# Optimization experiments

Hardware: AMD Instinct MI355X
Metric: run time of the kernel (lower is better)

The kernel has to match this reference:

```python
import jax, jax.numpy as jnp
import numpy as np

B, T, D_MODEL = 2, 2048, 2048
N_HEAD, N_KV, HD = 32, 8, 64


def _rope_tables(T, hd, base=10000.0):
    # standard rotary tables, (T, hd) with frequencies repeated over both halves
    inv_freq = 1.0 / (base ** (np.arange(0, hd // 2, dtype=np.float32) / (hd // 2)))
    t = np.arange(T, dtype=np.float32)
    freqs = np.outer(t, inv_freq)            # (T, hd/2)
    emb = np.concatenate([freqs, freqs], axis=-1)  # (T, hd)
    return jnp.asarray(np.cos(emb)), jnp.asarray(np.sin(emb))


def setup_inputs() -> dict:
    key = jax.random.key(0)
    ks = jax.random.split(key, 5)
    cos, sin = _rope_tables(T, HD)
    s = 0.02
    return {
        "x": jax.random.normal(ks[0], (B, T, D_MODEL), jnp.float32),
        "cos": cos,
        "sin": sin,
        "Wq": jax.random.normal(ks[1], (N_HEAD * HD, D_MODEL), jnp.float32) * s,
        "Wk": jax.random.normal(ks[2], (N_KV * HD, D_MODEL), jnp.float32) * s,
        "Wv": jax.random.normal(ks[3], (N_KV * HD, D_MODEL), jnp.float32) * s,
        "Wo": jax.random.normal(ks[4], (D_MODEL, N_HEAD * HD), jnp.float32) * s,
    }


def _apply_rope(x, cos, sin):
    # x: (B, H, T, D); cos/sin: (T, D)
    D = x.shape[-1]
    x1, x2 = x[..., : D // 2], x[..., D // 2 :]
    rot = jnp.concatenate([-x2, x1], axis=-1)
    c = cos[: x.shape[-2]][None, None]
    s = sin[: x.shape[-2]][None, None]
    return x * c + rot * s


def reference(x, cos, sin, Wq, Wk, Wv, Wo):
    Bv, Tv, _ = x.shape
    q = (x @ Wq.T).reshape(Bv, Tv, N_HEAD, HD).transpose(0, 2, 1, 3)  # (B,H,T,D)
    k = (x @ Wk.T).reshape(Bv, Tv, N_KV, HD).transpose(0, 2, 1, 3)    # (B,Hkv,T,D)
    v = (x @ Wv.T).reshape(Bv, Tv, N_KV, HD).transpose(0, 2, 1, 3)
    q = _apply_rope(q, cos, sin)
    k = _apply_rope(k, cos, sin)
    repeat = N_HEAD // N_KV
    if repeat > 1:
        k = jnp.repeat(k, repeat, axis=1)
        v = jnp.repeat(v, repeat, axis=1)
    scale = 1.0 / jnp.sqrt(jnp.float32(HD)).astype(x.dtype)
    scores = jnp.einsum("bhqd,bhkd->bhqk", q, k) * scale
    causal = jnp.tril(jnp.ones((Tv, Tv), dtype=bool))
    scores = jnp.where(causal[None, None], scores, jnp.finfo(scores.dtype).min)
    attn = jax.nn.softmax(scores, axis=-1)
    out = jnp.einsum("bhqk,bhkd->bhqd", attn, v)
    out = out.transpose(0, 2, 1, 3).reshape(Bv, Tv, N_HEAD * HD)
    return out @ Wo.T
```

## Files before the change

kernel.cpp:

```cpp
#include <hip/hip_runtime.h>
#include <stdint.h>

#define B_SZ 2
#define T_SEQ 2048
#define DM 2048
#define NH 32
#define NKV 8
#define HD 64
#define QKV_W 3072

typedef unsigned short u16;
typedef __bf16 bf16x8 __attribute__((ext_vector_type(8)));
typedef float floatx4 __attribute__((ext_vector_type(4)));

__device__ __forceinline__ float bf2f(u16 u) {
  union { unsigned u; float f; } v; v.u = ((unsigned)u) << 16; return v.f;
}
__device__ __forceinline__ u16 f2bf(float f) {
  union { float f; unsigned u; } v; v.f = f;
  unsigned r = v.u + 0x7fff + ((v.u >> 16) & 1);
  return (u16)(r >> 16);
}
__device__ __forceinline__ unsigned pk2bf(float hi, float lo) {
  return __builtin_amdgcn_perm(__float_as_uint(hi), __float_as_uint(lo), 0x07060302u);
}
__device__ __forceinline__ float fexp2(float x) {
#if __has_builtin(__builtin_amdgcn_exp2f)
  return __builtin_amdgcn_exp2f(x);
#else
  return exp2f(x);
#endif
}

__device__ __forceinline__ void gld_lds16(const void* g, void* l) {
  __builtin_amdgcn_global_load_lds(
      (const __attribute__((address_space(1))) unsigned int*)g,
      (__attribute__((address_space(3))) unsigned int*)l, 16, 0, 0);
}

__global__ __launch_bounds__(256) void conv_kernel(
    const float* __restrict__ src, u16* __restrict__ dst, int n4)
{
  int i = blockIdx.x * 256 + threadIdx.x;
  int stride = gridDim.x * 256;
  for (; i < n4; i += stride) {
    float4 v = ((const float4*)src)[i];
    ushort4 o;
    o.x = f2bf(v.x); o.y = f2bf(v.y); o.z = f2bf(v.z); o.w = f2bf(v.w);
    ((ushort4*)dst)[i] = o;
  }
}

__global__ __launch_bounds__(256) void gemm_qkv_kernel(
    const u16* __restrict__ A, const u16* __restrict__ Bt,
    u16* __restrict__ C)
{
  __shared__ __align__(16) u16 sA[128 * 32];
  __shared__ __align__(16) u16 sB[128 * 32];

  const int n0 = blockIdx.x * 128;
  const int m0 = blockIdx.y * 128;
  const int K = 2048;

  const int tid  = threadIdx.x;
  const int lane = tid & 63;
  const int w    = tid >> 6;
  const int wm = w >> 1, wn = w & 1;
  const int lm = lane & 15, lq = lane >> 4;

  floatx4 acc[4][4];
  #pragma unroll
  for (int i = 0; i < 4; i++)
    #pragma unroll
    for (int j = 0; j < 4; j++) { floatx4 z = {0.f,0.f,0.f,0.f}; acc[i][j] = z; }

  const int ar = tid >> 2;
  const int ac = (tid & 3) * 8;
  const u16* Ap0 = A  + (size_t)(m0 + ar) * K + ac;
  const u16* Ap1 = A  + (size_t)(m0 + 64 + ar) * K + ac;
  const u16* Bp0 = Bt + (size_t)(n0 + ar) * K + ac;
  const u16* Bp1 = Bt + (size_t)(n0 + 64 + ar) * K + ac;
  u16* sAd = sA + tid * 8;
  u16* sBd = sB + tid * 8;

  for (int k0 = 0; k0 < K; k0 += 32) {
    gld_lds16(Ap0 + k0, sAd);
    gld_lds16(Ap1 + k0, sAd + 2048);
    gld_lds16(Bp0 + k0, sBd);
    gld_lds16(Bp1 + k0, sBd + 2048);
    __syncthreads();

    bf16x8 af[4], bfr[4];
    #pragma unroll
    for (int mi = 0; mi < 4; mi++)
      af[mi] = *(const bf16x8*)(sA + (wm*64 + mi*16 + lm)*32 + lq*8);
    #pragma unroll
    for (int ni = 0; ni < 4; ni++)
      bfr[ni] = *(const bf16x8*)(sB + (wn*64 + ni*16 + lm)*32 + lq*8);

    #pragma unroll
    for (int mi = 0; mi < 4; mi++)
      #pragma unroll
      for (int ni = 0; ni < 4; ni++)
        acc[mi][ni] = __builtin_amdgcn_mfma_f32_16x16x32_bf16(
            af[mi], bfr[ni], acc[mi][ni], 0, 0, 0);
    __syncthreads();
  }

  #pragma unroll
  for (int mi = 0; mi < 4; mi++)
    #pragma unroll
    for (int ni = 0; ni < 4; ni++)
      #pragma unroll
      for (int r = 0; r < 4; r++) {
        int row = m0 + wm*64 + mi*16 + lq*4 + r;
        int col = n0 + wn*64 + ni*16 + lm;
        C[(size_t)row * QKV_W + col] = f2bf(acc[mi][ni][r]);
      }
}

__global__ __launch_bounds__(256) void gemm_out_kernel(
    const u16* __restrict__ A, const u16* __restrict__ Bt,
    float* __restrict__ C)
{
  __shared__ __align__(16) u16 sA[128 * 32];
  __shared__ __align__(16) u16 sB[128 * 32];

  const int n0 = blockIdx.x * 128;
  const int m0 = blockIdx.y * 128;
  const int K = 2048;

  const int tid  = threadIdx.x;
  const int lane = tid & 63;
  const int w    = tid >> 6;
  const int wm = w >> 1, wn = w & 1;
  const int lm = lane & 15, lq = lane >> 4;

  floatx4 acc[4][4];
  #pragma unroll
  for (int i = 0; i < 4; i++)
    #pragma unroll
    for (int j = 0; j < 4; j++) { floatx4 z = {0.f,0.f,0.f,0.f}; acc[i][j] = z; }

  const int ar = tid >> 2;
  const int ac = (tid & 3) * 8;
  const u16* Ap0 = A  + (size_t)(m0 + ar) * K + ac;
  const u16* Ap1 = A  + (size_t)(m0 + 64 + ar) * K + ac;
  const u16* Bp0 = Bt + (size_t)(n0 + ar) * K + ac;
  const u16* Bp1 = Bt + (size_t)(n0 + 64 + ar) * K + ac;
  u16* sAd = sA + tid * 8;
  u16* sBd = sB + tid * 8;

  for (int k0 = 0; k0 < K; k0 += 32) {
    gld_lds16(Ap0 + k0, sAd);
    gld_lds16(Ap1 + k0, sAd + 2048);
    gld_lds16(Bp0 + k0, sBd);
    gld_lds16(Bp1 + k0, sBd + 2048);
    __syncthreads();

    bf16x8 af[4], bfr[4];
    #pragma unroll
    for (int mi = 0; mi < 4; mi++)
      af[mi] = *(const bf16x8*)(sA + (wm*64 + mi*16 + lm)*32 + lq*8);
    #pragma unroll
    for (int ni = 0; ni < 4; ni++)
      bfr[ni] = *(const bf16x8*)(sB + (wn*64 + ni*16 + lm)*32 + lq*8);

    #pragma unroll
    for (int mi = 0; mi < 4; mi++)
      #pragma unroll
      for (int ni = 0; ni < 4; ni++)
        acc[mi][ni] = __builtin_amdgcn_mfma_f32_16x16x32_bf16(
            af[mi], bfr[ni], acc[mi][ni], 0, 0, 0);
    __syncthreads();
  }

  #pragma unroll
  for (int mi = 0; mi < 4; mi++)
    #pragma unroll
    for (int ni = 0; ni < 4; ni++)
      #pragma unroll
      for (int r = 0; r < 4; r++) {
        int row = m0 + wm*64 + mi*16 + lq*4 + r;
        int col = n0 + wn*64 + ni*16 + lm;
        C[(size_t)row * DM + col] = acc[mi][ni][r];
      }
}

#define QSCALE 0.180336880f
__global__ __launch_bounds__(256) void rope_kernel(
    const u16* __restrict__ qkv, const float* __restrict__ cosf,
    const float* __restrict__ sinf, u16* __restrict__ qb, u16* __restrict__ kb)
{
  const int bt = blockIdx.x;
  const int b = bt / T_SEQ, t = bt % T_SEQ;
  const int tid = threadIdx.x;
  const u16* row = qkv + (size_t)bt * QKV_W;

  #pragma unroll
  for (int i = 0; i < 4; i++) {
    int idx = i * 256 + tid;
    int h = idx >> 5, dp = idx & 31;
    float x1 = bf2f(row[h * 64 + dp]);
    float x2 = bf2f(row[h * 64 + dp + 32]);
    float c = cosf[t * 64 + dp];
    float s = sinf[t * 64 + dp];
    float o1 = (x1 * c - x2 * s) * QSCALE;
    float o2 = (x2 * c + x1 * s) * QSCALE;
    size_t base = ((size_t)(b * NH + h) * T_SEQ + t) * HD + dp;
    qb[base]      = f2bf(o1);
    qb[base + 32] = f2bf(o2);
  }
  {
    int idx = tid;
    int kvh = idx >> 5, dp = idx & 31;
    float x1 = bf2f(row[2048 + kvh * 64 + dp]);
    float x2 = bf2f(row[2048 + kvh * 64 + dp + 32]);
    float c = cosf[t * 64 + dp];
    float s = sinf[t * 64 + dp];
    size_t base = ((size_t)(b * NKV + kvh) * T_SEQ + t) * HD + dp;
    kb[base]      = f2bf(x1 * c - x2 * s);
    kb[base + 32] = f2bf(x2 * c + x1 * s);
  }
}

__global__ __launch_bounds__(256) void vtrans_kernel(
    const u16* __restrict__ qkv, u16* __restrict__ vbt)
{
  __shared__ u16 tile[64][66];
  const int t0  = blockIdx.x * 64;
  const int kvh = blockIdx.y;
  const int b   = blockIdx.z;
  const int tid = threadIdx.x;

  #pragma unroll
  for (int i = 0; i < 16; i++) {
    int idx = i * 256 + tid;
    int r = idx >> 6, c = idx & 63;
    tile[r][c] = qkv[(size_t)(b * T_SEQ + t0 + r) * QKV_W + 2560 + kvh * 64 + c];
  }
  __syncthreads();
  #pragma unroll
  for (int i = 0; i < 16; i++) {
    int idx = i * 256 + tid;
    int d = idx >> 6, c = idx & 63;
    vbt[((size_t)(b * NKV + kvh) * HD + d) * T_SEQ + t0 + c] = tile[c][d];
  }
}

__global__ __launch_bounds__(256, 2) void attn_kernel(
    const u16* __restrict__ qb, const u16* __restrict__ kb,
    const u16* __restrict__ vbt, u16* __restrict__ attn)
{
  __shared__ __align__(16) u16 sK[64 * 64];
  __shared__ __align__(16) u16 sV[64 * 64];
  __shared__ __align__(16) u16 sP[4][16][72];
  __shared__ float sAl[4][16];

  const int tid  = threadIdx.x;
  const int lane = tid & 63;
  const int w    = tid >> 6;

  const int l  = blockIdx.x;
  const int qt = 63 - (l >> 4);
  const int kv = l & 7;
  const int b  = (l >> 3) & 1;
  const int h  = kv * 4 + w;
  const int ktmax = qt >> 1;
  const int moff  = 32 * (qt & 1);

  const int lm = lane & 15, lq = lane >> 4;
  const int sw = lm & 7;

  bf16x8 qf[2][2];
  {
    const u16* qhead = qb + ((size_t)(b * NH + h) * T_SEQ + qt * 32) * HD;
    #pragma unroll
    for (int nq = 0; nq < 2; nq++) {
      const u16* qrow = qhead + (size_t)(nq * 16 + lm) * HD + lq * 8;
      qf[nq][0] = *(const bf16x8*)(qrow);
      qf[nq][1] = *(const bf16x8*)(qrow + 32);
    }
  }

  floatx4 o_acc[2][4];
  #pragma unroll
  for (int i = 0; i < 2; i++)
    #pragma unroll
    for (int j = 0; j < 4; j++) { floatx4 z = {0.f,0.f,0.f,0.f}; o_acc[i][j] = z; }
  float m_run[2] = {-1e30f, -1e30f};
  float l_run[2] = {0.f, 0.f};

  const u16* kbase = kb  + (size_t)(b * NKV + kv) * T_SEQ * HD;
  const u16* vbase = vbt + (size_t)(b * NKV + kv) * HD * T_SEQ;

  const int p0row = tid >> 3,        p1row = (256 + tid) >> 3;
  const int p0ck  = (tid & 7) ^ (p0row & 7), p1ck = ((256 + tid) & 7) ^ (p1row & 7);
  const u16* kp0 = kbase + (size_t)p0row * HD + p0ck * 8;
  const u16* kp1 = kbase + (size_t)p1row * HD + p1ck * 8;
  const u16* vp0 = vbase + (size_t)p0row * T_SEQ + p0ck * 8;
  const u16* vp1 = vbase + (size_t)p1row * T_SEQ + p1ck * 8;
  char* sKd0 = (char*)sK + tid * 16;        char* sKd1 = (char*)sK + (256 + tid) * 16;
  char* sVd0 = (char*)sV + tid * 16;        char* sVd1 = (char*)sV + (256 + tid) * 16;

  for (int kt = 0; kt <= ktmax; kt++) {
    __syncthreads();
    gld_lds16(kp0 + (size_t)kt * 64 * HD, sKd0);
    gld_lds16(kp1 + (size_t)kt * 64 * HD, sKd1);
    gld_lds16(vp0 + kt * 64, sVd0);
    gld_lds16(vp1 + kt * 64, sVd1);
    __syncthreads();

    bf16x8 kf[4][2], vf[4][2];
    #pragma unroll
    for (int nt = 0; nt < 4; nt++) {
      kf[nt][0] = *(const bf16x8*)(sK + (((nt*16 + lm) * 8 + (lq ^ sw)) << 3));
      kf[nt][1] = *(const bf16x8*)(sK + (((nt*16 + lm) * 8 + ((4 + lq) ^ sw)) << 3));
      vf[nt][0] = *(const bf16x8*)(sV + (((nt*16 + lm) * 8 + (lq ^ sw)) << 3));
      vf[nt][1] = *(const bf16x8*)(sV + (((nt*16 + lm) * 8 + ((4 + lq) ^ sw)) << 3));
    }

    #pragma unroll
    for (int nq = 0; nq < 2; nq++) {
      floatx4 s_acc[4];
      #pragma unroll
      for (int nt = 0; nt < 4; nt++) {
        floatx4 z = {0.f,0.f,0.f,0.f};
        z = __builtin_amdgcn_mfma_f32_16x16x32_bf16(kf[nt][0], qf[nq][0], z, 0, 0, 0);
        z = __builtin_amdgcn_mfma_f32_16x16x32_bf16(kf[nt][1], qf[nq][1], z, 0, 0, 0);
        s_acc[nt] = z;
      }

      if (kt == ktmax) {
        #pragma unroll
        for (int nt = 0; nt < 4; nt++)
          #pragma unroll
          for (int r = 0; r < 4; r++)
            if (nt * 16 + lq * 4 + r > nq * 16 + lm + moff) s_acc[nt][r] = -1e30f;
      }

      float mloc = s_acc[0][0];
      #pragma unroll
      for (int nt = 0; nt < 4; nt++)
        #pragma unroll
        for (int r = 0; r < 4; r++) mloc = fmaxf(mloc, s_acc[nt][r]);
      mloc = fmaxf(mloc, __shfl_xor(mloc, 16));
      mloc = fmaxf(mloc, __shfl_xor(mloc, 32));
      float mnew = fmaxf(m_run[nq], mloc);
      float al = fexp2(m_run[nq] - mnew);

      float rs = 0.f;
      uint2 pk[4];
      #pragma unroll
      for (int nt = 0; nt < 4; nt++) {
        float p0 = fexp2(s_acc[nt][0] - mnew);
        float p1 = fexp2(s_acc[nt][1] - mnew);
        float p2 = fexp2(s_acc[nt][2] - mnew);
        float p3 = fexp2(s_acc[nt][3] - mnew);
        rs += (p0 + p1) + (p2 + p3);
        pk[nt].x = pk2bf(p1, p0);
        pk[nt].y = pk2bf(p3, p2);
      }
      rs += __shfl_xor(rs, 16);
      rs += __shfl_xor(rs, 32);
      l_run[nq] = l_run[nq] * al + rs;
      m_run[nq] = mnew;

      #pragma unroll
      for (int nt = 0; nt < 4; nt++)
        *(uint2*)&sP[w][lm][nt * 16 + lq * 4] = pk[nt];

      if (lq == 0) sAl[w][lm] = al;
      floatx4 alv = *(const floatx4*)&sAl[w][lq * 4];
      #pragma unroll
      for (int nd = 0; nd < 4; nd++)
        #pragma unroll
        for (int r = 0; r < 4; r++)
          o_acc[nq][nd][r] *= alv[r];

      #pragma unroll
      for (int st = 0; st < 2; st++) {
        bf16x8 pf = *(const bf16x8*)(&sP[w][lm][st * 32 + lq * 8]);
        #pragma unroll
        for (int nd = 0; nd < 4; nd++)
          o_acc[nq][nd] = __builtin_amdgcn_mfma_f32_16x16x32_bf16(
              pf, vf[nd][st], o_acc[nq][nd], 0, 0, 0);
      }
    }
  }

  #pragma unroll
  for (int nq = 0; nq < 2; nq++) {
    __builtin_amdgcn_s_waitcnt(0);
    if (lq == 0) sAl[w][lm] = l_run[nq];
    floatx4 lv = *(const floatx4*)&sAl[w][lq * 4];
    #pragma unroll
    for (int nd = 0; nd < 4; nd++)
      #pragma unroll
      for (int r = 0; r < 4; r++) {
        float v = o_acc[nq][nd][r] / lv[r];
        size_t row = (size_t)b * T_SEQ + qt * 32 + nq * 16 + lq * 4 + r;
        attn[row * DM + h * HD + nd * 16 + lm] = f2bf(v);
      }
  }
}

extern "C" void kernel_launch(void* const* d_in, const int* in_sizes, int n_in,
                              void* d_out, int out_size, void* d_ws, size_t ws_size,
                              hipStream_t stream)
{
  const float* x    = (const float*)d_in[0];
  const float* cosf = (const float*)d_in[1];
  const float* sinf = (const float*)d_in[2];
  const float* Wq   = (const float*)d_in[3];
  const float* Wk   = (const float*)d_in[4];
  const float* Wv   = (const float*)d_in[5];
  const float* Wo   = (const float*)d_in[6];
  float* out = (float*)d_out;

  char* ws = (char*)d_ws;
  u16* qkvb  = (u16*)(ws + 0);
  u16* attnb = (u16*)(ws + 0);
  u16* qb    = (u16*)(ws + 25165824);
  u16* kb    = (u16*)(ws + 41943040);
  u16* vbt   = (u16*)(ws + 46137344);
  u16* xb    = (u16*)(ws + 50331648);
  u16* wob   = (u16*)(ws + 50331648);
  u16* wqkvb = (u16*)(ws + 67108864);

  dim3 blk(256);
  conv_kernel<<<dim3(2048), blk, 0, stream>>>(x,  xb,                 8388608 / 4);
  conv_kernel<<<dim3(1024), blk, 0, stream>>>(Wq, wqkvb,              4194304 / 4);
  conv_kernel<<<dim3(512),  blk, 0, stream>>>(Wk, wqkvb + 2048*2048,  1048576 / 4);
  conv_kernel<<<dim3(512),  blk, 0, stream>>>(Wv, wqkvb + 2560*2048,  1048576 / 4);

  gemm_qkv_kernel<<<dim3(24, 32), blk, 0, stream>>>(xb, wqkvb, qkvb);

  conv_kernel<<<dim3(1024), blk, 0, stream>>>(Wo, wob, 4194304 / 4);

  rope_kernel<<<dim3(B_SZ * T_SEQ), blk, 0, stream>>>(qkvb, cosf, sinf, qb, kb);
  vtrans_kernel<<<dim3(T_SEQ / 64, NKV, B_SZ), blk, 0, stream>>>(qkvb, vbt);
  attn_kernel<<<dim3(1024), blk, 0, stream>>>(qb, kb, vbt, attnb);
  gemm_out_kernel<<<dim3(16, 32), blk, 0, stream>>>(attnb, wob, out);
}
```

Baseline: 317.5 us.

## Double-buffer K/V tiles, add lazy softmax rescaling and MFMA priority hints

Splits the K/V shared-memory tiles into two buffers so the next tile's global-to-LDS load is issued while the current tile is computed, which removes the second barrier per iteration. Online-softmax rescaling of the output accumulator is skipped unless the row max grows by more than a threshold across the wave. It also raises wave priority around the MFMA blocks and raises the occupancy hint in launch bounds. The cost is doubled LDS for K/V and possible register pressure, and correctness of the double buffer relies on the direct-to-LDS loads being complete before the single barrier at the top of the next iteration.

```diff
diff --git a/kernel.cpp b/kernel.cpp
--- a/kernel.cpp
+++ b/kernel.cpp
@@ -248,12 +248,12 @@
   }
 }
 
-__global__ __launch_bounds__(256, 2) void attn_kernel(
+__global__ __launch_bounds__(256, 3) void attn_kernel(
     const u16* __restrict__ qb, const u16* __restrict__ kb,
     const u16* __restrict__ vbt, u16* __restrict__ attn)
 {
-  __shared__ __align__(16) u16 sK[64 * 64];
-  __shared__ __align__(16) u16 sV[64 * 64];
+  __shared__ __align__(16) u16 sK[2][64 * 64];
+  __shared__ __align__(16) u16 sV[2][64 * 64];
   __shared__ __align__(16) u16 sP[4][16][72];
   __shared__ float sAl[4][16];
 
@@ -300,29 +300,43 @@
   const u16* kp1 = kbase + (size_t)p1row * HD + p1ck * 8;
   const u16* vp0 = vbase + (size_t)p0row * T_SEQ + p0ck * 8;
   const u16* vp1 = vbase + (size_t)p1row * T_SEQ + p1ck * 8;
-  char* sKd0 = (char*)sK + tid * 16;        char* sKd1 = (char*)sK + (256 + tid) * 16;
-  char* sVd0 = (char*)sV + tid * 16;        char* sVd1 = (char*)sV + (256 + tid) * 16;
+  char* sKb = (char*)sK;
+  char* sVb = (char*)sV;
+  const int d0 = tid * 16, d1 = (256 + tid) * 16;
+
+  gld_lds16(kp0, sKb + d0);
+  gld_lds16(kp1, sKb + d1);
+  gld_lds16(vp0, sVb + d0);
+  gld_lds16(vp1, sVb + d1);
 
   for (int kt = 0; kt <= ktmax; kt++) {
     __syncthreads();
-    gld_lds16(kp0 + (size_t)kt * 64 * HD, sKd0);
-    gld_lds16(kp1 + (size_t)kt * 64 * HD, sKd1);
-    gld_lds16(vp0 + kt * 64, sVd0);
-    gld_lds16(vp1 + kt * 64, sVd1);
-    __syncthreads();
+    const int cur = kt & 1;
+    if (kt < ktmax) {
+      const int nb = (cur ^ 1) * 8192;
+      const size_t ko = (size_t)(kt + 1) * 64 * HD;
+      const int vo = (kt + 1) * 64;
+      gld_lds16(kp0 + ko, sKb + nb + d0);
+      gld_lds16(kp1 + ko, sKb + nb + d1);
+      gld_lds16(vp0 + vo, sVb + nb + d0);
+      gld_lds16(vp1 + vo, sVb + nb + d1);
+    }
+    const u16* sKc = sK[cur];
+    const u16* sVc = sV[cur];
 
     bf16x8 kf[4][2], vf[4][2];
     #pragma unroll
     for (int nt = 0; nt < 4; nt++) {
-      kf[nt][0] = *(const bf16x8*)(sK + (((nt*16 + lm) * 8 + (lq ^ sw)) << 3));
-      kf[nt][1] = *(const bf16x8*)(sK + (((nt*16 + lm) * 8 + ((4 + lq) ^ sw)) << 3));
-      vf[nt][0] = *(const bf16x8*)(sV + (((nt*16 + lm) * 8 + (lq ^ sw)) << 3));
-      vf[nt][1] = *(const bf16x8*)(sV + (((nt*16 + lm) * 8 + ((4 + lq) ^ sw)) << 3));
+      kf[nt][0] = *(const bf16x8*)(sKc + (((nt*16 + lm) * 8 + (lq ^ sw)) << 3));
+      kf[nt][1] = *(const bf16x8*)(sKc + (((nt*16 + lm) * 8 + ((4 + lq) ^ sw)) << 3));
+      vf[nt][0] = *(const bf16x8*)(sVc + (((nt*16 + lm) * 8 + (lq ^ sw)) << 3));
+      vf[nt][1] = *(const bf16x8*)(sVc + (((nt*16 + lm) * 8 + ((4 + lq) ^ sw)) << 3));
     }
 
     #pragma unroll
     for (int nq = 0; nq < 2; nq++) {
       floatx4 s_acc[4];
+      __builtin_amdgcn_s_setprio(1);
       #pragma unroll
       for (int nt = 0; nt < 4; nt++) {
         floatx4 z = {0.f,0.f,0.f,0.f};
@@ -330,6 +344,7 @@
         z = __builtin_amdgcn_mfma_f32_16x16x32_bf16(kf[nt][1], qf[nq][1], z, 0, 0, 0);
         s_acc[nt] = z;
       }
+      __builtin_amdgcn_s_setprio(0);
 
       if (kt == ktmax) {
         #pragma unroll
@@ -346,8 +361,21 @@
         for (int r = 0; r < 4; r++) mloc = fmaxf(mloc, s_acc[nt][r]);
       mloc = fmaxf(mloc, __shfl_xor(mloc, 16));
       mloc = fmaxf(mloc, __shfl_xor(mloc, 32));
-      float mnew = fmaxf(m_run[nq], mloc);
-      float al = fexp2(m_run[nq] - mnew);
+
+      float mnew = m_run[nq];
+      if (!__all(mloc - m_run[nq] <= 8.0f)) {
+        mnew = fmaxf(m_run[nq], mloc);
+        float al = fexp2(m_run[nq] - mnew);
+        m_run[nq] = mnew;
+        l_run[nq] *= al;
+        if (lq == 0) sAl[w][lm] = al;
+        floatx4 alv = *(const floatx4*)&sAl[w][lq * 4];
+        #pragma unroll
+        for (int nd = 0; nd < 4; nd++)
+          #pragma unroll
+          for (int r = 0; r < 4; r++)
+            o_acc[nq][nd][r] *= alv[r];
+      }
 
       float rs = 0.f;
       uint2 pk[4];
@@ -363,21 +391,13 @@
       }
       rs += __shfl_xor(rs, 16);
       rs += __shfl_xor(rs, 32);
-      l_run[nq] = l_run[nq] * al + rs;
-      m_run[nq] = mnew;
+      l_run[nq] += rs;
 
       #pragma unroll
       for (int nt = 0; nt < 4; nt++)
         *(uint2*)&sP[w][lm][nt * 16 + lq * 4] = pk[nt];
 
-      if (lq == 0) sAl[w][lm] = al;
-      floatx4 alv = *(const floatx4*)&sAl[w][lq * 4];
-      #pragma unroll
-      for (int nd = 0; nd < 4; nd++)
-        #pragma unroll
-        for (int r = 0; r < 4; r++)
-          o_acc[nq][nd][r] *= alv[r];
-
+      __builtin_amdgcn_s_setprio(1);
       #pragma unroll
       for (int st = 0; st < 2; st++) {
         bf16x8 pf = *(const bf16x8*)(&sP[w][lm][st * 32 + lq * 8]);
@@ -386,6 +406,7 @@
           o_acc[nq][nd] = __builtin_amdgcn_mfma_f32_16x16x32_bf16(
               pf, vf[nd][st], o_acc[nq][nd], 0, 0, 0);
       }
+      __builtin_amdgcn_s_setprio(0);
     }
   }
 
```

New measurement: 311.2 us. 1.02x faster.
